# Kernel tuning notes

Measured on AMD Instinct MI355X. Metric: run time of the kernel, lower is better.

## Reference

```python
import jax, jax.numpy as jnp
import numpy as np

INPUT_DIM = 512
HIDDEN_DIM = 512
B, N = 8, 2048


def setup_inputs() -> dict:
    key = jax.random.key(0)
    ks = jax.random.split(key, 9)
    s_in = 1.0 / np.sqrt(INPUT_DIM)
    s_h = 1.0 / np.sqrt(HIDDEN_DIM)
    return {
        "X": jax.random.normal(ks[0], (B, N, INPUT_DIM), dtype=jnp.float32),
        "Wq": jax.random.uniform(ks[1], (INPUT_DIM, HIDDEN_DIM), minval=-s_in, maxval=s_in),
        "bq": jnp.zeros((HIDDEN_DIM,), jnp.float32),
        "Wk": jax.random.uniform(ks[2], (INPUT_DIM, HIDDEN_DIM), minval=-s_in, maxval=s_in),
        "bk": jnp.zeros((HIDDEN_DIM,), jnp.float32),
        "Wv": jax.random.uniform(ks[3], (INPUT_DIM, HIDDEN_DIM), minval=-s_in, maxval=s_in),
        "bv": jnp.zeros((HIDDEN_DIM,), jnp.float32),
        "Wo": jax.random.uniform(ks[4], (HIDDEN_DIM, INPUT_DIM), minval=-s_h, maxval=s_h),
        "bo": jnp.zeros((INPUT_DIM,), jnp.float32),
        "ln_gamma": jnp.ones((INPUT_DIM,), jnp.float32),
        "ln_beta": jnp.zeros((INPUT_DIM,), jnp.float32),
    }


def reference(X, Wq, bq, Wk, bk, Wv, bv, Wo, bo, ln_gamma, ln_beta):
    q = X @ Wq + bq                      # [B,N,H]
    k = X @ Wk + bk
    v = X @ Wv + bv
    scores = jnp.einsum('bnh,bmh->bnm', q, k) / jnp.sqrt(jnp.float32(HIDDEN_DIM))
    attn = jax.nn.softmax(scores, axis=-1)      # [B,N,N]
    ctx = jnp.einsum('bnm,bmh->bnh', attn, v)   # [B,N,H]
    out = ctx @ Wo + bo + X                      # residual
    mu = jnp.mean(out, axis=-1, keepdims=True)
    var = jnp.var(out, axis=-1, keepdims=True)
    normed = (out - mu) / jnp.sqrt(var + 1e-5)
    return normed * ln_gamma + ln_beta
```

## Files before the change

kernel.cpp:

```cpp
#include <hip/hip_runtime.h>
#include <cstdint>
#include <cstddef>


typedef __bf16 bf16x8 __attribute__((ext_vector_type(8)));
typedef float  f32x4  __attribute__((ext_vector_type(4)));

__device__ __forceinline__ uint16_t f2bf(float f) {
  union { float f; uint32_t u; } v; v.f = f;
  uint32_t r = v.u + 0x7FFFu + ((v.u >> 16) & 1u);
  return (uint16_t)(r >> 16);
}

__device__ __forceinline__ void gld16(const uint16_t* g, uint16_t* l) {
  __builtin_amdgcn_global_load_lds(
      (__attribute__((address_space(1))) void*)(g),
      (__attribute__((address_space(3))) void*)(l), 16, 0, 0);
}

__global__ __launch_bounds__(256, 1) void attn_k(
    const uint16_t* __restrict__ qg, const uint16_t* __restrict__ kg,
    const uint16_t* __restrict__ vTg, uint16_t* __restrict__ ctx,
    float scale) {
  __shared__ alignas(16) uint16_t Ks[64 * 512];
  __shared__ alignas(16) uint16_t Vs[512 * 64];
  __shared__ alignas(16) uint16_t Es[64 * 64];
  __shared__ float rs[64][2];

  const int tid = threadIdx.x;
  const int w = tid >> 6, lane = tid & 63;
  const int wm = w >> 1, wn = w & 1;
  const int lr = lane & 15, q4 = lane >> 4;
  const int lr7 = lr & 7;
  const int l3 = lane >> 3, l7 = lane & 7;

  const int hw = blockIdx.x + 32 * blockIdx.y;
  const int lg = (hw & 7) * 32 + (hw >> 3);
  const int bx = lg & 31, z = lg >> 5;
  const int q0 = bx * 64;

  const uint16_t* qb = qg + ((size_t)z * 2048 + q0) * 512;
  const uint16_t* kb = kg + (size_t)z * 2048 * 512;
  const uint16_t* vb = vTg + (size_t)z * 512 * 2048;

  bf16x8 qf[2][16];
#pragma unroll
  for (int mt = 0; mt < 2; mt++)
#pragma unroll
    for (int ks = 0; ks < 16; ks++)
      qf[mt][ks] = *(const bf16x8*)&qb[(size_t)(wm * 32 + mt * 16 + lr) * 512 +
                                       ks * 32 + q4 * 8];
  asm volatile("s_waitcnt vmcnt(0)" ::: "memory");

  f32x4 acc[4][8];
#pragma unroll
  for (int mt = 0; mt < 4; mt++)
#pragma unroll
    for (int ht = 0; ht < 8; ht++) acc[mt][ht] = (f32x4){0.f, 0.f, 0.f, 0.f};
  float psum[2][4] = {{0.f, 0.f, 0.f, 0.f}, {0.f, 0.f, 0.f, 0.f}};

  for (int kt = 0; kt < 32; ++kt) {
    const int kv0 = kt * 64;
#pragma unroll
    for (int j = 0; j < 16; j++) {
      const int r = w * 16 + j;
      gld16(kb + (size_t)(kv0 + r) * 512 + (lane ^ (r & 7)) * 8, &Ks[r * 512]);
    }
#pragma unroll
    for (int j = 0; j < 16; j++) {
      const int g = w * 16 + j;
      gld16(vb + (size_t)(g * 8 + l3) * 2048 + kv0 + (l7 ^ l3) * 8,
            &Vs[g * 512]);
    }
    asm volatile("s_waitcnt vmcnt(16)" ::: "memory");
    __builtin_amdgcn_s_barrier();

    f32x4 sacc[2][2];
#pragma unroll
    for (int mt = 0; mt < 2; mt++)
#pragma unroll
      for (int nt = 0; nt < 2; nt++) sacc[mt][nt] = (f32x4){0.f, 0.f, 0.f, 0.f};
#pragma unroll
    for (int ks = 0; ks < 16; ks++) {
      bf16x8 kf[2];
#pragma unroll
      for (int nt = 0; nt < 2; nt++) {
        const int r = wn * 32 + nt * 16 + lr;
        kf[nt] = *(const bf16x8*)&Ks[r * 512 + ((ks * 4 + q4) ^ lr7) * 8];
      }
#pragma unroll
      for (int nt = 0; nt < 2; nt++)
#pragma unroll
        for (int mt = 0; mt < 2; mt++)
          sacc[mt][nt] = __builtin_amdgcn_mfma_f32_16x16x32_bf16(
              qf[mt][ks], kf[nt], sacc[mt][nt], 0, 0, 0);
    }
#pragma unroll
    for (int mt = 0; mt < 2; mt++)
#pragma unroll
      for (int nt = 0; nt < 2; nt++)
#pragma unroll
        for (int i = 0; i < 4; i++) {
          const float e = __expf(sacc[mt][nt][i] * scale);
          const int r = wm * 32 + mt * 16 + q4 * 4 + i;
          const int c = wn * 32 + nt * 16 + lr;
          Es[r * 64 + (((c >> 3) ^ (r & 7)) * 8) + lr7] = f2bf(e);
          psum[mt][i] += e;
        }
    asm volatile("s_waitcnt lgkmcnt(0)" ::: "memory");
    asm volatile("s_waitcnt vmcnt(0)" ::: "memory");
    __builtin_amdgcn_s_barrier();

#pragma unroll
    for (int ks = 0; ks < 2; ks++) {
      bf16x8 ef[4];
#pragma unroll
      for (int mt = 0; mt < 4; mt++)
        ef[mt] = *(const bf16x8*)&Es[(mt * 16 + lr) * 64 +
                                     ((ks * 4 + q4) ^ lr7) * 8];
#pragma unroll
      for (int ht = 0; ht < 8; ht++) {
        const int h = w * 128 + ht * 16 + lr;
        const bf16x8 vf =
            *(const bf16x8*)&Vs[h * 64 + ((ks * 4 + q4) ^ lr7) * 8];
#pragma unroll
        for (int mt = 0; mt < 4; mt++)
          acc[mt][ht] = __builtin_amdgcn_mfma_f32_16x16x32_bf16(
              ef[mt], vf, acc[mt][ht], 0, 0, 0);
      }
    }
    __builtin_amdgcn_s_barrier();
  }

#pragma unroll
  for (int mt = 0; mt < 2; mt++)
#pragma unroll
    for (int i = 0; i < 4; i++) {
      float p = psum[mt][i];
      p += __shfl_xor(p, 1); p += __shfl_xor(p, 2);
      p += __shfl_xor(p, 4); p += __shfl_xor(p, 8);
      if (lr == 0) rs[wm * 32 + mt * 16 + q4 * 4 + i][wn] = p;
    }
  __syncthreads();

#pragma unroll
  for (int mt = 0; mt < 4; mt++)
#pragma unroll
    for (int i = 0; i < 4; i++) {
      const int r = mt * 16 + q4 * 4 + i;
      const float inv = 1.0f / (rs[r][0] + rs[r][1]);
#pragma unroll
      for (int ht = 0; ht < 8; ht++) {
        const int col = w * 128 + ht * 16 + lr;
        ctx[((size_t)z * 2048 + q0 + r) * 512 + col] =
            f2bf(acc[mt][ht][i] * inv);
      }
    }
}

template <int BM, int BN>
__global__ __launch_bounds__(256, 2) void gemm_k(
    const uint16_t* __restrict__ A, const uint16_t* __restrict__ Bt,
    uint16_t* __restrict__ OutQ, uint16_t* __restrict__ OutK,
    uint16_t* __restrict__ OutVT, int K, int lda, int ldb,
    const float* __restrict__ b0, const float* __restrict__ b1,
    const float* __restrict__ b2) {
  constexpr int MT = BM / 32;
  constexpr int NT = BN / 32;
  constexpr int AI = BM / 64;
  constexpr int BI = BN / 64;
  constexpr int PW = AI + BI;
  __shared__ alignas(16) uint16_t As[3][BM * 32];
  __shared__ alignas(16) uint16_t Bs[3][BN * 32];

  const int tid = threadIdx.x;
  const int w = tid >> 6, lane = tid & 63;
  const int wm = w >> 1, wn = w & 1;

  const int gx = gridDim.x, gy = gridDim.y;
  const int nwg = gx * gy;
  const int hw = blockIdx.x + gx * blockIdx.y;
  const int lg = (hw & 7) * (nwg >> 3) + (hw >> 3);
  const int bx = lg % gx, by = lg / gx;

  const int m0 = by * BM, n0 = bx * BN;

  const int kc = (((lane & 3) ^ ((lane >> 2) & 3) ^ (lane >> 4)) * 8);
  const int rbA = w * (BM / 4);
  const int rbB = w * (BN / 4);
  const uint16_t* gA = A + (size_t)(m0 + rbA + (lane >> 2)) * lda + kc;
  const uint16_t* gB = Bt + (size_t)(n0 + rbB + (lane >> 2)) * ldb + kc;

  f32x4 acc[MT][NT];
#pragma unroll
  for (int i = 0; i < MT; i++)
#pragma unroll
    for (int j = 0; j < NT; j++) acc[i][j] = (f32x4){0.f, 0.f, 0.f, 0.f};

  const int lr = lane & 15, q4 = lane >> 4;
  const int swz = (((lane >> 4) ^ (lr & 3) ^ (lr >> 2)) * 8);
  const int iters = K >> 5;

  auto stage = [&](int t, int buf) {
    const int k0 = t * 32;
#pragma unroll
    for (int j = 0; j < AI; j++)
      gld16(gA + k0 + (size_t)(j * 16) * lda, &As[buf][(rbA + j * 16) * 32]);
#pragma unroll
    for (int j = 0; j < BI; j++)
      gld16(gB + k0 + (size_t)(j * 16) * ldb, &Bs[buf][(rbB + j * 16) * 32]);
  };

  auto compute = [&](int buf) {
    bf16x8 af[MT], bfr[NT];
#pragma unroll
    for (int t = 0; t < MT; t++)
      af[t] = *(const bf16x8*)&As[buf][(wm * (BM / 2) + t * 16 + lr) * 32 + swz];
#pragma unroll
    for (int t = 0; t < NT; t++)
      bfr[t] = *(const bf16x8*)&Bs[buf][(wn * (BN / 2) + t * 16 + lr) * 32 + swz];
#pragma unroll
    for (int nt = 0; nt < NT; nt++)
#pragma unroll
      for (int mt = 0; mt < MT; mt++)
        acc[mt][nt] = __builtin_amdgcn_mfma_f32_16x16x32_bf16(
            af[mt], bfr[nt], acc[mt][nt], 0, 0, 0);
  };

  stage(0, 0);
  stage(1, 1);
  int buf = 0;
  for (int i = 0; i < iters - 1; ++i) {
    asm volatile("s_waitcnt vmcnt(%0)" ::"i"(PW) : "memory");
    __builtin_amdgcn_s_barrier();
    if (i + 2 < iters) stage(i + 2, (buf + 2 >= 3) ? buf - 1 : buf + 2);
    compute(buf);
    buf = (buf == 2) ? 0 : buf + 1;
  }
  asm volatile("s_waitcnt vmcnt(0)" ::: "memory");
  __builtin_amdgcn_s_barrier();
  compute(buf);

#pragma unroll
  for (int mt = 0; mt < MT; mt++) {
#pragma unroll
    for (int nt = 0; nt < NT; nt++) {
#pragma unroll
      for (int i = 0; i < 4; i++) {
        const int row = m0 + wm * (BM / 2) + mt * 16 + q4 * 4 + i;
        const int col = n0 + wn * (BN / 2) + nt * 16 + lr;
        const float v = acc[mt][nt][i];
        const int which = col >> 9, c = col & 511;
        if (which == 0) {
          OutQ[(size_t)row * 512 + c] = f2bf(v + b0[c]);
        } else if (which == 1) {
          OutK[(size_t)row * 512 + c] = f2bf(v + b1[c]);
        } else {
          OutVT[(size_t)(row >> 11) * (512 * 2048) + (size_t)c * 2048 +
                (row & 2047)] = f2bf(v + b2[c]);
        }
      }
    }
  }
}

template <int BM, int BN, int WM, int WN>
__global__ __launch_bounds__(512, 4) void gemmf_k(
    const uint16_t* __restrict__ A, const uint16_t* __restrict__ Bt,
    void* __restrict__ OutA, int K, int lda, int ldb,
    const float* __restrict__ b0, const float* __restrict__ b1,
    const float* __restrict__ b2, const float* __restrict__ Xres) {
  constexpr int MT = (BM / WM) / 16;
  constexpr int NT = (BN / WN) / 16;
  static_assert(MT == 4 && NT == 4, "wave tile must be 64x64");
  constexpr int AI = (BM >= 128) ? BM / 128 : 1;
  constexpr int BI = BN / 128;
  constexpr int PW = AI + BI;
  __shared__ alignas(16) uint16_t As[3][BM * 32];
  __shared__ alignas(16) uint16_t Bs[3][BN * 32];

  const int tid = threadIdx.x;
  const int w = tid >> 6, lane = tid & 63;
  const int wm = w / WN, wn = w % WN;

  const int gx = gridDim.x, gy = gridDim.y;
  const int nwg = gx * gy;
  const int hw = blockIdx.x + gx * blockIdx.y;
  const int lg = (hw & 7) * (nwg >> 3) + (hw >> 3);
  const int bx = lg % gx, by = lg / gx;

  const int m0 = by * BM, n0 = bx * BN;

  const int kc = (((lane & 3) ^ ((lane >> 2) & 3) ^ (lane >> 4)) * 8);
  const int rbA = (BM >= 128) ? w * (BM / 8) : (w & 3) * 16;
  const int rbB = w * (BN / 8);
  const uint16_t* gA = A + (size_t)(m0 + rbA + (lane >> 2)) * lda + kc;
  const uint16_t* gB = Bt + (size_t)(n0 + rbB + (lane >> 2)) * ldb + kc;

  f32x4 acc[MT][NT];
#pragma unroll
  for (int i = 0; i < MT; i++)
#pragma unroll
    for (int j = 0; j < NT; j++) acc[i][j] = (f32x4){0.f, 0.f, 0.f, 0.f};

  const int lr = lane & 15, q4 = lane >> 4;
  const int swz = (((lane >> 4) ^ (lr & 3) ^ (lr >> 2)) * 8);
  const int iters = K >> 5;

  auto stage = [&](int t, int buf) {
    const int k0 = t * 32;
#pragma unroll
    for (int j = 0; j < AI; j++)
      gld16(gA + k0 + (size_t)(j * 16) * lda, &As[buf][(rbA + j * 16) * 32]);
#pragma unroll
    for (int j = 0; j < BI; j++)
      gld16(gB + k0 + (size_t)(j * 16) * ldb, &Bs[buf][(rbB + j * 16) * 32]);
  };

  auto compute = [&](int buf) {
    bf16x8 af[MT], bfr[NT];
#pragma unroll
    for (int t = 0; t < MT; t++)
      af[t] = *(const bf16x8*)&As[buf][(wm * (BM / WM) + t * 16 + lr) * 32 + swz];
#pragma unroll
    for (int t = 0; t < NT; t++)
      bfr[t] = *(const bf16x8*)&Bs[buf][(wn * (BN / WN) + t * 16 + lr) * 32 + swz];
#pragma unroll
    for (int nt = 0; nt < NT; nt++)
#pragma unroll
      for (int mt = 0; mt < MT; mt++)
        acc[mt][nt] = __builtin_amdgcn_mfma_f32_16x16x32_bf16(
            af[mt], bfr[nt], acc[mt][nt], 0, 0, 0);
  };

  stage(0, 0);
  stage(1, 1);
  int buf = 0;
  for (int i = 0; i < iters - 1; ++i) {
    asm volatile("s_waitcnt vmcnt(%0)" ::"i"(PW) : "memory");
    __builtin_amdgcn_s_barrier();
    if (i + 2 < iters) stage(i + 2, (buf + 2 >= 3) ? buf - 1 : buf + 2);
    compute(buf);
    buf = (buf == 2) ? 0 : buf + 1;
  }
  asm volatile("s_waitcnt vmcnt(0)" ::: "memory");
  __builtin_amdgcn_s_barrier();
  compute(buf);

  __shared__ float redS[8][64];
  __shared__ float redQ[8][64];
  float* Op = (float*)OutA;
  __syncthreads();
#pragma unroll
  for (int mt = 0; mt < MT; mt++) {
#pragma unroll
    for (int i = 0; i < 4; i++) {
      const int rl = mt * 16 + q4 * 4 + i;
      const int row = m0 + rl;
      float ps = 0.f, pq = 0.f;
#pragma unroll
      for (int nt = 0; nt < NT; nt++) {
        const int col = wn * 64 + nt * 16 + lr;
        float v = acc[mt][nt][i] + b0[col] + Xres[(size_t)row * 512 + col];
        acc[mt][nt][i] = v;
        ps += v; pq += v * v;
      }
      ps += __shfl_xor(ps, 1); pq += __shfl_xor(pq, 1);
      ps += __shfl_xor(ps, 2); pq += __shfl_xor(pq, 2);
      ps += __shfl_xor(ps, 4); pq += __shfl_xor(pq, 4);
      ps += __shfl_xor(ps, 8); pq += __shfl_xor(pq, 8);
      if (lr == 0) { redS[w][rl] = ps; redQ[w][rl] = pq; }
    }
  }
  __syncthreads();
#pragma unroll
  for (int mt = 0; mt < MT; mt++) {
#pragma unroll
    for (int i = 0; i < 4; i++) {
      const int rl = mt * 16 + q4 * 4 + i;
      const int row = m0 + rl;
      float s8 = 0.f, q8 = 0.f;
#pragma unroll
      for (int ww = 0; ww < 8; ww++) { s8 += redS[ww][rl]; q8 += redQ[ww][rl]; }
      const float mean = s8 * (1.f / 512.f);
      const float var = q8 * (1.f / 512.f) - mean * mean;
      const float rstd = rsqrtf(var + 1e-5f);
#pragma unroll
      for (int nt = 0; nt < NT; nt++) {
        const int col = wn * 64 + nt * 16 + lr;
        Op[(size_t)row * 512 + col] =
            (acc[mt][nt][i] - mean) * rstd * b1[col] + b2[col];
      }
    }
  }
}

__global__ __launch_bounds__(256) void cvt_all_k(
    const float* __restrict__ X, uint16_t* __restrict__ Xb,
    const float* __restrict__ Wq, const float* __restrict__ Wk,
    const float* __restrict__ Wv, const float* __restrict__ Wo,
    uint16_t* __restrict__ Wt) {
  const int i = blockIdx.x * 256 + threadIdx.x;
  const float4 f = ((const float4*)X)[i];
  uint32_t lo = (uint32_t)f2bf(f.x) | ((uint32_t)f2bf(f.y) << 16);
  uint32_t hi = (uint32_t)f2bf(f.z) | ((uint32_t)f2bf(f.w) << 16);
  ((uint2*)Xb)[i] = make_uint2(lo, hi);
  if (i < 2048 * 512) {
    const int n = i >> 9, kk = i & 511;
    const int which = n >> 9, c = n & 511;
    const float* W =
        (which == 0) ? Wq : (which == 1) ? Wk : (which == 2) ? Wv : Wo;
    Wt[i] = f2bf(W[kk * 512 + c]);
  }
}

extern "C" void kernel_launch(void* const* d_in, const int* in_sizes, int n_in,
                              void* d_out, int out_size, void* d_ws,
                              size_t ws_size, hipStream_t stream) {
  const float* X     = (const float*)d_in[0];
  const float* Wq    = (const float*)d_in[1];
  const float* bq    = (const float*)d_in[2];
  const float* Wk    = (const float*)d_in[3];
  const float* bk    = (const float*)d_in[4];
  const float* Wv    = (const float*)d_in[5];
  const float* bv    = (const float*)d_in[6];
  const float* Wo    = (const float*)d_in[7];
  const float* bo    = (const float*)d_in[8];
  const float* gamma = (const float*)d_in[9];
  const float* beta  = (const float*)d_in[10];
  float* out = (float*)d_out;

  char* ws = (char*)d_ws;
  uint16_t* Xb   = (uint16_t*)(ws);
  uint16_t* Wt   = (uint16_t*)(ws + 67108864);
  uint16_t* q    = (uint16_t*)(ws + 69206016);
  uint16_t* kb   = (uint16_t*)(ws + 85983232);
  uint16_t* vT   = (uint16_t*)(ws + 102760448);
  uint16_t* ctx  = q;

  ctx = Xb;

  cvt_all_k<<<dim3(8192), dim3(256), 0, stream>>>(X, Xb, Wq, Wk, Wv, Wo, Wt);
  gemm_k<128, 128><<<dim3(12, 128), dim3(256), 0, stream>>>(
      Xb, Wt, q, kb, vT, 512, 512, 512, bq, bk, bv);
  attn_k<<<dim3(32, 8), dim3(256), 0, stream>>>(
      q, kb, vT, ctx, 0.044194173824159216f);
  gemmf_k<64, 512, 1, 8><<<dim3(1, 256), dim3(512), 0, stream>>>(
      ctx, Wt + 1536 * 512, (void*)out, 512, 512, 512, bo, gamma, beta, X);
}
```

Before: 325.9 us.

## Double-buffer K/V tiles in attention and widen block to 512 threads

The attention kernel moves from 256 to 512 threads per block and shrinks the KV tile from 64 to 32 rows. K and V tiles are now double-buffered in shared memory, so the global-to-LDS loads for the next tile are issued before computing on the current one. Per-wave work is halved: one 16x16 score tile and a 64-column context slice per wave. This is meant to hide memory latency and raise the number of waves per CU. In exchange it doubles the loop iterations and barrier count, and each barrier now synchronises more waves.

```diff
diff --git a/kernel.cpp b/kernel.cpp
--- a/kernel.cpp
+++ b/kernel.cpp
@@ -18,21 +18,20 @@
       (__attribute__((address_space(3))) void*)(l), 16, 0, 0);
 }
 
-__global__ __launch_bounds__(256, 1) void attn_k(
+__global__ __launch_bounds__(512, 1) void attn_k(
     const uint16_t* __restrict__ qg, const uint16_t* __restrict__ kg,
     const uint16_t* __restrict__ vTg, uint16_t* __restrict__ ctx,
     float scale) {
-  __shared__ alignas(16) uint16_t Ks[64 * 512];
-  __shared__ alignas(16) uint16_t Vs[512 * 64];
-  __shared__ alignas(16) uint16_t Es[64 * 64];
+  __shared__ alignas(16) uint16_t Ks[2][32 * 512];
+  __shared__ alignas(16) uint16_t Vs[2][512 * 32];
+  __shared__ alignas(16) uint16_t Es[64 * 32];
   __shared__ float rs[64][2];
 
   const int tid = threadIdx.x;
   const int w = tid >> 6, lane = tid & 63;
   const int wm = w >> 1, wn = w & 1;
   const int lr = lane & 15, q4 = lane >> 4;
-  const int lr7 = lr & 7;
-  const int l3 = lane >> 3, l7 = lane & 7;
+  const int lr7 = lr & 7, lr3 = lr & 3;
 
   const int hw = blockIdx.x + 32 * blockIdx.y;
   const int lg = (hw & 7) * 32 + (hw >> 3);
@@ -43,104 +42,97 @@
   const uint16_t* kb = kg + (size_t)z * 2048 * 512;
   const uint16_t* vb = vTg + (size_t)z * 512 * 2048;
 
-  bf16x8 qf[2][16];
-#pragma unroll
-  for (int mt = 0; mt < 2; mt++)
-#pragma unroll
-    for (int ks = 0; ks < 16; ks++)
-      qf[mt][ks] = *(const bf16x8*)&qb[(size_t)(wm * 32 + mt * 16 + lr) * 512 +
-                                       ks * 32 + q4 * 8];
+  bf16x8 qf[16];
+#pragma unroll
+  for (int ks = 0; ks < 16; ks++)
+    qf[ks] = *(const bf16x8*)&qb[(size_t)(wm * 16 + lr) * 512 + ks * 32 +
+                                 q4 * 8];
   asm volatile("s_waitcnt vmcnt(0)" ::: "memory");
 
-  f32x4 acc[4][8];
+  f32x4 acc[4][4];
 #pragma unroll
   for (int mt = 0; mt < 4; mt++)
 #pragma unroll
-    for (int ht = 0; ht < 8; ht++) acc[mt][ht] = (f32x4){0.f, 0.f, 0.f, 0.f};
-  float psum[2][4] = {{0.f, 0.f, 0.f, 0.f}, {0.f, 0.f, 0.f, 0.f}};
-
-  for (int kt = 0; kt < 32; ++kt) {
-    const int kv0 = kt * 64;
-#pragma unroll
-    for (int j = 0; j < 16; j++) {
-      const int r = w * 16 + j;
-      gld16(kb + (size_t)(kv0 + r) * 512 + (lane ^ (r & 7)) * 8, &Ks[r * 512]);
-    }
-#pragma unroll
-    for (int j = 0; j < 16; j++) {
-      const int g = w * 16 + j;
-      gld16(vb + (size_t)(g * 8 + l3) * 2048 + kv0 + (l7 ^ l3) * 8,
-            &Vs[g * 512]);
-    }
-    asm volatile("s_waitcnt vmcnt(16)" ::: "memory");
+    for (int ht = 0; ht < 4; ht++) acc[mt][ht] = (f32x4){0.f, 0.f, 0.f, 0.f};
+  float psum[4] = {0.f, 0.f, 0.f, 0.f};
+
+  auto stageK = [&](int t, int b) {
+#pragma unroll
+    for (int j = 0; j < 4; j++) {
+      const int r = w * 4 + j;
+      gld16(kb + (size_t)(t * 32 + r) * 512 + (lane ^ (r & 7)) * 8,
+            &Ks[b][r * 512]);
+    }
+  };
+  auto stageV = [&](int t, int b) {
+#pragma unroll
+    for (int j = 0; j < 4; j++) {
+      const int g = w * 4 + j;
+      gld16(vb + (size_t)(g * 16 + (lane >> 2)) * 2048 + t * 32 +
+                (((lane & 3) ^ ((lane >> 2) & 3)) * 8),
+            &Vs[b][g * 16 * 32]);
+    }
+  };
+
+  stageK(0, 0);
+  stageV(0, 0);
+
+  for (int t = 0; t < 64; ++t) {
+    const int b = t & 1;
+    if (t + 1 < 64) {
+      stageK(t + 1, b ^ 1);
+      stageV(t + 1, b ^ 1);
+      asm volatile("s_waitcnt vmcnt(8)" ::: "memory");
+    } else {
+      asm volatile("s_waitcnt vmcnt(0)" ::: "memory");
+    }
     __builtin_amdgcn_s_barrier();
 
-    f32x4 sacc[2][2];
-#pragma unroll
-    for (int mt = 0; mt < 2; mt++)
-#pragma unroll
-      for (int nt = 0; nt < 2; nt++) sacc[mt][nt] = (f32x4){0.f, 0.f, 0.f, 0.f};
+    f32x4 sacc = (f32x4){0.f, 0.f, 0.f, 0.f};
 #pragma unroll
     for (int ks = 0; ks < 16; ks++) {
-      bf16x8 kf[2];
-#pragma unroll
-      for (int nt = 0; nt < 2; nt++) {
-        const int r = wn * 32 + nt * 16 + lr;
-        kf[nt] = *(const bf16x8*)&Ks[r * 512 + ((ks * 4 + q4) ^ lr7) * 8];
-      }
-#pragma unroll
-      for (int nt = 0; nt < 2; nt++)
-#pragma unroll
-        for (int mt = 0; mt < 2; mt++)
-          sacc[mt][nt] = __builtin_amdgcn_mfma_f32_16x16x32_bf16(
-              qf[mt][ks], kf[nt], sacc[mt][nt], 0, 0, 0);
-    }
-#pragma unroll
-    for (int mt = 0; mt < 2; mt++)
-#pragma unroll
-      for (int nt = 0; nt < 2; nt++)
-#pragma unroll
-        for (int i = 0; i < 4; i++) {
-          const float e = __expf(sacc[mt][nt][i] * scale);
-          const int r = wm * 32 + mt * 16 + q4 * 4 + i;
-          const int c = wn * 32 + nt * 16 + lr;
-          Es[r * 64 + (((c >> 3) ^ (r & 7)) * 8) + lr7] = f2bf(e);
-          psum[mt][i] += e;
-        }
+      const bf16x8 kf = *(const bf16x8*)
+          &Ks[b][(wn * 16 + lr) * 512 + (((ks * 4 + q4) ^ lr7) * 8)];
+      sacc = __builtin_amdgcn_mfma_f32_16x16x32_bf16(qf[ks], kf, sacc, 0, 0, 0);
+    }
+#pragma unroll
+    for (int i = 0; i < 4; i++) {
+      const float e = __expf(sacc[i] * scale);
+      const int r = wm * 16 + q4 * 4 + i;
+      const int c = wn * 16 + lr;
+      Es[r * 32 + (((c >> 3) ^ (r & 3)) * 8) + (c & 7)] = f2bf(e);
+      psum[i] += e;
+    }
     asm volatile("s_waitcnt lgkmcnt(0)" ::: "memory");
-    asm volatile("s_waitcnt vmcnt(0)" ::: "memory");
     __builtin_amdgcn_s_barrier();
 
-#pragma unroll
-    for (int ks = 0; ks < 2; ks++) {
-      bf16x8 ef[4];
+    bf16x8 ef[4];
+#pragma unroll
+    for (int mt = 0; mt < 4; mt++) {
+      const int rr = mt * 16 + lr;
+      ef[mt] = *(const bf16x8*)&Es[rr * 32 + ((q4 ^ lr3) * 8)];
+    }
+#pragma unroll
+    for (int ht = 0; ht < 4; ht++) {
+      const int h = w * 64 + ht * 16 + lr;
+      const bf16x8 vf = *(const bf16x8*)&Vs[b][h * 32 + ((q4 ^ lr3) * 8)];
 #pragma unroll
       for (int mt = 0; mt < 4; mt++)
-        ef[mt] = *(const bf16x8*)&Es[(mt * 16 + lr) * 64 +
-                                     ((ks * 4 + q4) ^ lr7) * 8];
-#pragma unroll
-      for (int ht = 0; ht < 8; ht++) {
-        const int h = w * 128 + ht * 16 + lr;
-        const bf16x8 vf =
-            *(const bf16x8*)&Vs[h * 64 + ((ks * 4 + q4) ^ lr7) * 8];
-#pragma unroll
-        for (int mt = 0; mt < 4; mt++)
-          acc[mt][ht] = __builtin_amdgcn_mfma_f32_16x16x32_bf16(
-              ef[mt], vf, acc[mt][ht], 0, 0, 0);
-      }
+        acc[mt][ht] = __builtin_amdgcn_mfma_f32_16x16x32_bf16(
+            ef[mt], vf, acc[mt][ht], 0, 0, 0);
     }
     __builtin_amdgcn_s_barrier();
   }
 
 #pragma unroll
-  for (int mt = 0; mt < 2; mt++)
-#pragma unroll
-    for (int i = 0; i < 4; i++) {
-      float p = psum[mt][i];
-      p += __shfl_xor(p, 1); p += __shfl_xor(p, 2);
-      p += __shfl_xor(p, 4); p += __shfl_xor(p, 8);
-      if (lr == 0) rs[wm * 32 + mt * 16 + q4 * 4 + i][wn] = p;
-    }
+  for (int i = 0; i < 4; i++) {
+    float p = psum[i];
+    p += __shfl_xor(p, 1); p += __shfl_xor(p, 2);
+    p += __shfl_xor(p, 4); p += __shfl_xor(p, 8);
+    if (lr == 0) {
+      rs[wm * 16 + q4 * 4 + i][wn] = p;
+    }
+  }
   __syncthreads();
 
 #pragma unroll
@@ -150,8 +142,8 @@
       const int r = mt * 16 + q4 * 4 + i;
       const float inv = 1.0f / (rs[r][0] + rs[r][1]);
 #pragma unroll
-      for (int ht = 0; ht < 8; ht++) {
-        const int col = w * 128 + ht * 16 + lr;
+      for (int ht = 0; ht < 4; ht++) {
+        const int col = w * 64 + ht * 16 + lr;
         ctx[((size_t)z * 2048 + q0 + r) * 512 + col] =
             f2bf(acc[mt][ht][i] * inv);
       }
@@ -436,14 +428,12 @@
   uint16_t* q    = (uint16_t*)(ws + 69206016);
   uint16_t* kb   = (uint16_t*)(ws + 85983232);
   uint16_t* vT   = (uint16_t*)(ws + 102760448);
-  uint16_t* ctx  = q;
-
-  ctx = Xb;
+  uint16_t* ctx  = Xb;
 
   cvt_all_k<<<dim3(8192), dim3(256), 0, stream>>>(X, Xb, Wq, Wk, Wv, Wo, Wt);
   gemm_k<128, 128><<<dim3(12, 128), dim3(256), 0, stream>>>(
       Xb, Wt, q, kb, vT, 512, 512, 512, bq, bk, bv);
-  attn_k<<<dim3(32, 8), dim3(256), 0, stream>>>(
+  attn_k<<<dim3(32, 8), dim3(512), 0, stream>>>(
       q, kb, vT, ctx, 0.044194173824159216f);
   gemmf_k<64, 512, 1, 8><<<dim3(1, 256), dim3(512), 0, stream>>>(
       ctx, Wt + 1536 * 512, (void*)out, 512, 512, 512, bo, gamma, beta, X);
```

Result: slower. 332.6 us (+2.0%).
